# Kernel tuning notes

Hardware: AMD Instinct MI355X
Metric: run time of the kernel (lower is better)

The kernel has to match this reference:

```python
import jax, jax.numpy as jnp
import numpy as np

D_MODEL = 1024
N_HEADS = 16
D_K = D_MODEL // N_HEADS
D_FF = 4096
EPS = 1e-6


def _layernorm(x, g, b):
    mu = jnp.mean(x, axis=-1, keepdims=True)
    var = jnp.mean(jnp.square(x - mu), axis=-1, keepdims=True)
    return (x - mu) * jax.lax.rsqrt(var + EPS) * g + b


def setup_inputs() -> dict:
    key = jax.random.key(0)
    ks = jax.random.split(key, 12)
    B, S = 2, 2048
    sd_attn = (1.0 / np.sqrt(2.0)) * np.sqrt(2.0 / (D_MODEL + D_MODEL))  # xavier gain 1/sqrt(2) (std approx)
    sd_ff1 = np.sqrt(2.0 / (D_MODEL + D_FF))
    sd_ff2 = np.sqrt(2.0 / (D_FF + D_MODEL))
    return {
        "x": jax.random.normal(ks[0], (B, S, D_MODEL), jnp.float32),
        "mask": jnp.ones((B, S), jnp.int32),
        # weights stored (in, out) so forward is x @ W
        "wq": jax.random.normal(ks[1], (D_MODEL, D_MODEL), jnp.float32) * sd_attn,
        "wk": jax.random.normal(ks[2], (D_MODEL, D_MODEL), jnp.float32) * sd_attn,
        "wv": jax.random.normal(ks[3], (D_MODEL, D_MODEL), jnp.float32) * sd_attn,
        "wo": jax.random.normal(ks[4], (D_MODEL, D_MODEL), jnp.float32) * sd_attn,
        "wo_b": jnp.zeros((D_MODEL,), jnp.float32),
        "w1": jax.random.normal(ks[5], (D_MODEL, D_FF), jnp.float32) * sd_ff1,
        "b1": jnp.zeros((D_FF,), jnp.float32),
        "w2": jax.random.normal(ks[6], (D_FF, D_MODEL), jnp.float32) * sd_ff2,
        "b2": jnp.zeros((D_MODEL,), jnp.float32),
        "g1": jnp.ones((D_MODEL,), jnp.float32),
        "be1": jnp.zeros((D_MODEL,), jnp.float32),
        "g2": jnp.ones((D_MODEL,), jnp.float32),
        "be2": jnp.zeros((D_MODEL,), jnp.float32),
    }


def reference(x, mask, wq, wk, wv, wo, wo_b, w1, b1, w2, b2, g1, be1, g2, be2):
    B, S, _ = x.shape
    scale = 1.0 / np.sqrt(D_K)
    # project and split heads -> [B, H, S, Dk]
    q = (x @ wq).reshape(B, S, N_HEADS, D_K).transpose(0, 2, 1, 3)
    k = (x @ wk).reshape(B, S, N_HEADS, D_K).transpose(0, 2, 1, 3)
    v = (x @ wv).reshape(B, S, N_HEADS, D_K).transpose(0, 2, 1, 3)
    scores = jnp.einsum("bhqd,bhkd->bhqk", q, k) * scale  # [B,H,S,S]
    m = (mask[:, None, None, :] == 0)
    scores = jnp.where(m, -1e9, scores)
    attn = jax.nn.softmax(scores, axis=-1)
    ctx = jnp.einsum("bhqk,bhkd->bhqd", attn, v)
    ctx = ctx.transpose(0, 2, 1, 3).reshape(B, S, D_MODEL)
    attn_out = ctx @ wo + wo_b
    x = _layernorm(x + attn_out, g1, be1)
    ff = jax.nn.gelu(x @ w1 + b1, approximate=False) @ w2 + b2
    return _layernorm(x + ff, g2, be2)
```

## Files before the change

kernel.cpp:

```cpp
#include <hip/hip_runtime.h>
#include <cstdint>

#define DEVINL __device__ __forceinline__

typedef __attribute__((ext_vector_type(8))) short short8;
typedef __attribute__((ext_vector_type(4))) float floatx4;
typedef __attribute__((ext_vector_type(4))) unsigned short ushort4v;

DEVINL unsigned short f2bf(float f) {
  union { float f; uint32_t u; } v; v.f = f;
  return (unsigned short)((v.u + 0x7fffu + ((v.u >> 16) & 1u)) >> 16);
}
DEVINL float bf2f(unsigned short h) {
  union { uint32_t u; float f; } v; v.u = ((uint32_t)h) << 16;
  return v.f;
}

#if defined(__has_builtin) && __has_builtin(__builtin_amdgcn_exp2f)
#define EXP2(x) __builtin_amdgcn_exp2f(x)
#else
#define EXP2(x) exp2f(x)
#endif

DEVINL float fast_gelu(float v) {
  const float z = -2.30220795f * v * (1.0f + 0.044715f * v * v);
  return v * __builtin_amdgcn_rcpf(1.0f + EXP2(z));
}

typedef __attribute__((address_space(3))) unsigned char* lds_ptr_t;
typedef const __attribute__((address_space(1))) unsigned char* gbl_ptr_t;
DEVINL void load_lds_128(const void* g, void* l) {
  __builtin_amdgcn_global_load_lds((gbl_ptr_t)g, (lds_ptr_t)l, 16, 0, 0);
}

#define MFMA16(a, b, c) __builtin_amdgcn_mfma_f32_16x16x32_bf16((a), (b), (c), 0, 0, 0)

#define QSCALE2 0.18033688011112042f

__global__ __launch_bounds__(256) void prep_kernel(
    const float* __restrict__ x, unsigned short* __restrict__ XB,
    const float* __restrict__ wq, const float* __restrict__ wk,
    const float* __restrict__ wv, const float* __restrict__ wo,
    unsigned short* __restrict__ WQKV, unsigned short* __restrict__ WOT,
    const float* __restrict__ w1, unsigned short* __restrict__ W1T,
    const float* __restrict__ w2, unsigned short* __restrict__ W2T) {
  const int bid = blockIdx.x;
  if (bid < 4096) {
    const int i = (bid * 256 + threadIdx.x) * 4;
    floatx4 v = *(const floatx4*)(x + i);
    ushort4v o;
#pragma unroll
    for (int j = 0; j < 4; ++j) o[j] = f2bf(v[j]);
    *(ushort4v*)(XB + i) = o;
    return;
  }
  const float* in;
  unsigned short* out;
  int K, N, bx, by;
  if (bid < 8192) {
    const int b2 = bid - 4096, z = b2 >> 10;
    in = (z == 0) ? wq : (z == 1) ? wk : (z == 2) ? wv : wo;
    out = (z == 3) ? WOT : WQKV + (size_t)z * 1024 * 1024;
    K = 1024; N = 1024; bx = b2 & 31; by = (b2 >> 5) & 31;
  } else if (bid < 12288) {
    const int b3 = bid - 8192;
    in = w1; out = W1T; K = 1024; N = 4096; bx = b3 & 127; by = b3 >> 7;
  } else {
    const int b4 = bid - 12288;
    in = w2; out = W2T; K = 4096; N = 1024; bx = b4 & 31; by = b4 >> 5;
  }
  __shared__ float tile[32][33];
  const int n0 = bx * 32, k0 = by * 32;
  const int tx = threadIdx.x & 31, ty = threadIdx.x >> 5;
#pragma unroll
  for (int i = 0; i < 4; ++i)
    tile[ty + 8 * i][tx] = in[(size_t)(k0 + ty + 8 * i) * N + n0 + tx];
  __syncthreads();
#pragma unroll
  for (int i = 0; i < 4; ++i)
    out[(size_t)(n0 + ty + 8 * i) * K + k0 + tx] = f2bf(tile[tx][ty + 8 * i]);
}

template <int EPI, int SK>
__global__ __launch_bounds__(256) void gemm_bt_kernel(
    const unsigned short* __restrict__ A, const unsigned short* __restrict__ BT,
    const float* __restrict__ bias, void* __restrict__ C0, void* __restrict__ C1,
    void* __restrict__ C2, int M, int N, int K) {
  __shared__ __align__(16) unsigned short As[128 * 64];
  __shared__ __align__(16) unsigned short Bs[128 * 64];
  const int tid = threadIdx.x;
  const int w = tid >> 6, l = tid & 63;
  const int lq = l >> 4, lr = l & 15;
  const int m0 = blockIdx.y * 128, n0 = blockIdx.x * 128;
  const int wm = (w >> 1) * 64, wn = (w & 1) * 64;
  const int r_a = l >> 2;
  const int colb = (l & 3) * 8;
  const int kslice = K / SK;
  const int kbeg = kslice * blockIdx.z;

  floatx4 acc[4][4];
  const floatx4 fz = {0.f, 0.f, 0.f, 0.f};
#pragma unroll
  for (int mt = 0; mt < 4; ++mt)
#pragma unroll
    for (int nt = 0; nt < 4; ++nt) acc[mt][nt] = fz;

  for (int k0 = kbeg; k0 < kbeg + kslice; k0 += 64) {
    __syncthreads();
#pragma unroll
    for (int p = 0; p < 2; ++p) {
#pragma unroll
      for (int i = 0; i < 2; ++i) {
        const int c = w * 2 + i;
        load_lds_128(A + (size_t)(m0 + c * 16 + r_a) * K + k0 + p * 32 + colb,
                     (char*)As + p * 8192 + c * 1024);
        load_lds_128(BT + (size_t)(n0 + c * 16 + r_a) * K + k0 + p * 32 + colb,
                     (char*)Bs + p * 8192 + c * 1024);
      }
    }
    __syncthreads();
#pragma unroll
    for (int p = 0; p < 2; ++p) {
      short8 af[4], bf[4];
#pragma unroll
      for (int mt = 0; mt < 4; ++mt)
        af[mt] = *(const short8*)((const char*)As + p * 8192 + (wm + mt * 16 + lr) * 64 + lq * 16);
#pragma unroll
      for (int nt = 0; nt < 4; ++nt)
        bf[nt] = *(const short8*)((const char*)Bs + p * 8192 + (wn + nt * 16 + lr) * 64 + lq * 16);
#pragma unroll
      for (int mt = 0; mt < 4; ++mt)
#pragma unroll
        for (int nt = 0; nt < 4; ++nt)
          acc[mt][nt] = MFMA16(af[mt], bf[nt], acc[mt][nt]);
    }
  }

  void* Cp = (SK > 1 && blockIdx.z) ? C1 : C0;
#pragma unroll
  for (int mt = 0; mt < 4; ++mt) {
#pragma unroll
    for (int nt = 0; nt < 4; ++nt) {
      const int n = n0 + wn + nt * 16 + lr;
      float bval = 0.f;
      if (EPI == 2) bval = bias[n];
#pragma unroll
      for (int r = 0; r < 4; ++r) {
        const int m = m0 + wm + mt * 16 + lq * 4 + r;
        float v = acc[mt][nt][r];
        if (EPI == 4) {
          ((unsigned short*)Cp)[(size_t)m * N + n] = f2bf(v);
        } else if (EPI == 2) {
          ((unsigned short*)C0)[(size_t)m * N + n] = f2bf(fast_gelu(v + bval));
        } else {
          const int reg = n >> 10;
          if (reg == 0) {
            ((unsigned short*)C0)[(size_t)m * 1024 + n] = f2bf(v * QSCALE2);
          } else if (reg == 1) {
            ((unsigned short*)C1)[(size_t)m * 1024 + (n - 1024)] = f2bf(v);
          } else {
            const int nn = n - 2048;
            const int bidx = m >> 11, s = m & 2047;
            const int hh = nn >> 6, d = nn & 63;
            ((unsigned short*)C2)[((size_t)((bidx * 16 + hh) * 64 + d)) * 2048 + s] = f2bf(v);
          }
        }
      }
    }
  }
}

__global__ __launch_bounds__(256, 4) void flash_kernel(
    const unsigned short* __restrict__ Q, const unsigned short* __restrict__ Kg,
    const unsigned short* __restrict__ VT, const int* __restrict__ mask,
    unsigned short* __restrict__ ctx) {
  __shared__ __align__(16) unsigned short Ks[128 * 64];
  __shared__ __align__(16) unsigned short VTs[64 * 128];
  __shared__ __align__(16) unsigned short PQ[64 * 64];

  const int tid = threadIdx.x, w = tid >> 6, l = tid & 63;
  const int lq = l >> 4, lr = l & 15;
  const int bh = blockIdx.y, b = bh >> 4, h = bh & 15;
  const int q0 = blockIdx.x * 64;

  const unsigned short* Qp = Q + (size_t)(b * 2048 + q0) * 1024 + h * 64;
  const unsigned short* Kp = Kg + (size_t)(b * 2048) * 1024 + h * 64;
  const unsigned short* VTp = VT + (size_t)bh * 64 * 2048;
  const int* mp = mask + b * 2048;

  {
    const int rq = l >> 3, cs = l & 7;
#pragma unroll
    for (int i = 0; i < 2; ++i) {
      const int c = w * 2 + i;
      load_lds_128(Qp + (size_t)(c * 8 + rq) * 1024 + cs * 8, (char*)PQ + c * 1024);
    }
  }
  __syncthreads();
  short8 qf[2];
  qf[0] = *(const short8*)((const char*)PQ + (w * 16 + lr) * 128 + lq * 16);
  qf[1] = *(const short8*)((const char*)PQ + (w * 16 + lr) * 128 + 64 + lq * 16);

  short8 ones;
#pragma unroll
  for (int j = 0; j < 8; ++j) ones[j] = (short)0x3F80;

  const floatx4 fz = {0.f, 0.f, 0.f, 0.f};
  floatx4 o[4] = {fz, fz, fz, fz};
  floatx4 l_acc = fz;

  const int krow = l >> 3, kslot = l & 7;
  const int vrow = l >> 4, vslot = l & 15;
  const int pswz = (lr >> 2) & 3;

  for (int kb = 0; kb < 2048; kb += 128) {
    __syncthreads();
#pragma unroll
    for (int i = 0; i < 4; ++i) {
      const int c4 = w * 4 + i;
      {
        const int row = c4 * 8 + krow;
        const int cc = kslot ^ (row & 7);
        load_lds_128(Kp + (size_t)(kb + row) * 1024 + cc * 8, (char*)Ks + c4 * 1024);
      }
      {
        const int row = c4 * 4 + vrow;
        const int cc = vslot ^ (row & 15);
        load_lds_128(VTp + (size_t)row * 2048 + kb + cc * 8, (char*)VTs + c4 * 1024);
      }
    }
    int msk[8];
#pragma unroll
    for (int g = 0; g < 8; ++g) msk[g] = mp[kb + g * 16 + lr];
    __syncthreads();

    floatx4 s[8];
#pragma unroll
    for (int g = 0; g < 8; ++g) {
      const char* rowp = (const char*)Ks + (g * 16 + lr) * 128;
      short8 k0 = *(const short8*)(rowp + ((lq) ^ (lr & 7)) * 16);
      short8 k1 = *(const short8*)(rowp + ((4 + lq) ^ (lr & 7)) * 16);
      floatx4 t = MFMA16(qf[0], k0, fz);
      s[g] = MFMA16(qf[1], k1, t);
    }

    float pH[4][4];
#pragma unroll
    for (int r = 0; r < 4; ++r) {
      unsigned short* pr = PQ + (w * 16 + lq * 4 + r) * 64;
#pragma unroll
      for (int g = 0; g < 4; ++g)
        pr[((g ^ lq) * 16) + lr] = f2bf(msk[g] ? EXP2(s[g][r]) : 0.f);
#pragma unroll
      for (int g = 0; g < 4; ++g)
        pH[r][g] = msk[4 + g] ? EXP2(s[4 + g][r]) : 0.f;
    }

#pragma unroll
    for (int t = 0; t < 2; ++t) {
      short8 pf = *(const short8*)((const char*)PQ + (w * 16 + lr) * 128 +
                                   (((t * 32 + lq * 8) ^ (pswz * 16)) * 2));
      l_acc = MFMA16(pf, ones, l_acc);
#pragma unroll
      for (int nt = 0; nt < 4; ++nt) {
        short8 vf = *(const short8*)((const char*)VTs + (nt * 16 + lr) * 256 +
                                     ((t * 4 + lq) ^ lr) * 16);
        o[nt] = MFMA16(pf, vf, o[nt]);
      }
    }
#pragma unroll
    for (int r = 0; r < 4; ++r) {
      unsigned short* pr = PQ + (w * 16 + lq * 4 + r) * 64;
#pragma unroll
      for (int g = 0; g < 4; ++g) pr[((g ^ lq) * 16) + lr] = f2bf(pH[r][g]);
    }
#pragma unroll
    for (int t = 0; t < 2; ++t) {
      short8 pf = *(const short8*)((const char*)PQ + (w * 16 + lr) * 128 +
                                   (((t * 32 + lq * 8) ^ (pswz * 16)) * 2));
      l_acc = MFMA16(pf, ones, l_acc);
#pragma unroll
      for (int nt = 0; nt < 4; ++nt) {
        short8 vf = *(const short8*)((const char*)VTs + (nt * 16 + lr) * 256 +
                                     ((8 + t * 4 + lq) ^ lr) * 16);
        o[nt] = MFMA16(pf, vf, o[nt]);
      }
    }
  }

#pragma unroll
  for (int r = 0; r < 4; ++r) {
    const float inv = 1.0f / l_acc[r];
    const int q = q0 + w * 16 + lq * 4 + r;
#pragma unroll
    for (int nt = 0; nt < 4; ++nt)
      ctx[(size_t)(b * 2048 + q) * 1024 + h * 64 + nt * 16 + lr] = f2bf(o[nt][r] * inv);
  }
}

template <int RESBF, int OUTBF>
__global__ __launch_bounds__(256) void ln2_kernel(
    const void* __restrict__ res, const unsigned short* __restrict__ y0,
    const unsigned short* __restrict__ y1, const float* __restrict__ bias,
    const float* __restrict__ gamma, const float* __restrict__ beta,
    void* __restrict__ outp) {
  const int row = blockIdx.x, t = threadIdx.x;
  const size_t base = (size_t)row * 1024 + t * 4;
  float v[4];
  if (RESBF) {
    ushort4v r4 = *(const ushort4v*)((const unsigned short*)res + base);
#pragma unroll
    for (int j = 0; j < 4; ++j) v[j] = bf2f(r4[j]);
  } else {
    floatx4 r4 = *(const floatx4*)((const float*)res + base);
#pragma unroll
    for (int j = 0; j < 4; ++j) v[j] = r4[j];
  }
  const ushort4v a4 = *(const ushort4v*)(y0 + base);
  const ushort4v b4v = *(const ushort4v*)(y1 + base);
  const floatx4 bi4 = *(const floatx4*)(bias + t * 4);
  float s = 0.f, ss = 0.f;
#pragma unroll
  for (int j = 0; j < 4; ++j) {
    v[j] += bf2f(a4[j]) + bf2f(b4v[j]) + bi4[j];
    s += v[j];
    ss += v[j] * v[j];
  }
#pragma unroll
  for (int off = 1; off < 64; off <<= 1) {
    s += __shfl_xor(s, off);
    ss += __shfl_xor(ss, off);
  }
  __shared__ float red[8];
  const int w = t >> 6;
  if ((t & 63) == 0) { red[w] = s; red[4 + w] = ss; }
  __syncthreads();
  s = red[0] + red[1] + red[2] + red[3];
  ss = red[4] + red[5] + red[6] + red[7];
  const float mean = s * (1.0f / 1024.0f);
  const float var = ss * (1.0f / 1024.0f) - mean * mean;
  const float rstd = rsqrtf(var + 1e-6f);
  const floatx4 g4 = *(const floatx4*)(gamma + t * 4);
  const floatx4 be4 = *(const floatx4*)(beta + t * 4);
  if (OUTBF) {
    ushort4v o;
#pragma unroll
    for (int j = 0; j < 4; ++j) o[j] = f2bf((v[j] - mean) * rstd * g4[j] + be4[j]);
    *(ushort4v*)((unsigned short*)outp + base) = o;
  } else {
    floatx4 o;
#pragma unroll
    for (int j = 0; j < 4; ++j) o[j] = (v[j] - mean) * rstd * g4[j] + be4[j];
    *(floatx4*)((float*)outp + base) = o;
  }
}

extern "C" void kernel_launch(void* const* d_in, const int* in_sizes, int n_in,
                              void* d_out, int out_size, void* d_ws, size_t ws_size,
                              hipStream_t stream) {
  (void)in_sizes; (void)n_in; (void)out_size; (void)ws_size;
  const float* x    = (const float*)d_in[0];
  const int*   mask = (const int*)d_in[1];
  const float* wq   = (const float*)d_in[2];
  const float* wk   = (const float*)d_in[3];
  const float* wv   = (const float*)d_in[4];
  const float* wo   = (const float*)d_in[5];
  const float* wo_b = (const float*)d_in[6];
  const float* w1   = (const float*)d_in[7];
  const float* b1   = (const float*)d_in[8];
  const float* w2   = (const float*)d_in[9];
  const float* b2   = (const float*)d_in[10];
  const float* g1   = (const float*)d_in[11];
  const float* be1  = (const float*)d_in[12];
  const float* g2   = (const float*)d_in[13];
  const float* be2  = (const float*)d_in[14];
  float* out = (float*)d_out;

  char* ws = (char*)d_ws;
  const size_t MB = 1024ull * 1024ull;
  unsigned short* WQKV = (unsigned short*)(ws + 0 * MB);
  unsigned short* WOT  = (unsigned short*)(ws + 6 * MB);
  unsigned short* W1T  = (unsigned short*)(ws + 8 * MB);
  unsigned short* W2T  = (unsigned short*)(ws + 16 * MB);
  unsigned short* XB   = (unsigned short*)(ws + 24 * MB);
  unsigned short* Qb   = (unsigned short*)(ws + 32 * MB);
  unsigned short* Kb   = (unsigned short*)(ws + 40 * MB);
  unsigned short* VTb  = (unsigned short*)(ws + 48 * MB);
  unsigned short* CTX  = (unsigned short*)(ws + 56 * MB);
  unsigned short* ATT0 = (unsigned short*)(ws + 32 * MB);
  unsigned short* ATT1 = (unsigned short*)(ws + 40 * MB);
  unsigned short* Hb   = (unsigned short*)(ws + 24 * MB);
  unsigned short* G1   = (unsigned short*)(ws + 32 * MB);
  unsigned short* FF20 = (unsigned short*)(ws + 64 * MB);
  unsigned short* FF21 = (unsigned short*)(ws + 72 * MB);

  prep_kernel<<<16384, 256, 0, stream>>>(x, XB, wq, wk, wv, wo, WQKV, WOT,
                                         w1, W1T, w2, W2T);
  gemm_bt_kernel<5, 1><<<dim3(24, 32), 256, 0, stream>>>(
      XB, WQKV, nullptr, Qb, Kb, VTb, 4096, 3072, 1024);
  flash_kernel<<<dim3(32, 32), 256, 0, stream>>>(Qb, Kb, VTb, mask, CTX);
  gemm_bt_kernel<4, 2><<<dim3(8, 32, 2), 256, 0, stream>>>(
      CTX, WOT, nullptr, ATT0, ATT1, nullptr, 4096, 1024, 1024);
  ln2_kernel<0, 1><<<4096, 256, 0, stream>>>(x, ATT0, ATT1, wo_b, g1, be1, Hb);
  gemm_bt_kernel<2, 1><<<dim3(32, 32), 256, 0, stream>>>(
      Hb, W1T, b1, G1, nullptr, nullptr, 4096, 4096, 1024);
  gemm_bt_kernel<4, 2><<<dim3(8, 32, 2), 256, 0, stream>>>(
      G1, W2T, nullptr, FF20, FF21, nullptr, 4096, 1024, 4096);
  ln2_kernel<1, 0><<<4096, 256, 0, stream>>>(Hb, FF20, FF21, b2, g2, be2, out);
}
```

Baseline: 366.2 us.

## Keep softmax probabilities in registers by transposing the score MFMA operands

Swaps the operand order of the QK^T MFMA so each lane's score accumulator already matches the A-operand layout the PV MFMA needs. The probabilities are packed into bf16 fragments in registers, which removes the LDS round trip through the PQ buffer. To fit the new fragment order, V^T is read as two 4-element pieces per fragment and the mask is loaded as int4 vectors. This cuts LDS traffic and shared memory use, but adds more, narrower LDS reads for V and extra register pressure.

```diff
diff --git a/kernel.cpp b/kernel.cpp
--- a/kernel.cpp
+++ b/kernel.cpp
@@ -4,6 +4,7 @@
 #define DEVINL __device__ __forceinline__
 
 typedef __attribute__((ext_vector_type(8))) short short8;
+typedef __attribute__((ext_vector_type(4))) short short4v;
 typedef __attribute__((ext_vector_type(4))) float floatx4;
 typedef __attribute__((ext_vector_type(4))) unsigned short ushort4v;
 
@@ -176,7 +177,6 @@
     unsigned short* __restrict__ ctx) {
   __shared__ __align__(16) unsigned short Ks[128 * 64];
   __shared__ __align__(16) unsigned short VTs[64 * 128];
-  __shared__ __align__(16) unsigned short PQ[64 * 64];
 
   const int tid = threadIdx.x, w = tid >> 6, l = tid & 63;
   const int lq = l >> 4, lr = l & 15;
@@ -193,13 +193,13 @@
 #pragma unroll
     for (int i = 0; i < 2; ++i) {
       const int c = w * 2 + i;
-      load_lds_128(Qp + (size_t)(c * 8 + rq) * 1024 + cs * 8, (char*)PQ + c * 1024);
+      load_lds_128(Qp + (size_t)(c * 8 + rq) * 1024 + cs * 8, (char*)Ks + c * 1024);
     }
   }
   __syncthreads();
   short8 qf[2];
-  qf[0] = *(const short8*)((const char*)PQ + (w * 16 + lr) * 128 + lq * 16);
-  qf[1] = *(const short8*)((const char*)PQ + (w * 16 + lr) * 128 + 64 + lq * 16);
+  qf[0] = *(const short8*)((const char*)Ks + (w * 16 + lr) * 128 + lq * 16);
+  qf[1] = *(const short8*)((const char*)Ks + (w * 16 + lr) * 128 + 64 + lq * 16);
 
   short8 ones;
 #pragma unroll
@@ -211,7 +211,6 @@
 
   const int krow = l >> 3, kslot = l & 7;
   const int vrow = l >> 4, vslot = l & 15;
-  const int pswz = (lr >> 2) & 3;
 
   for (int kb = 0; kb < 2048; kb += 128) {
     __syncthreads();
@@ -229,61 +228,52 @@
         load_lds_128(VTp + (size_t)row * 2048 + kb + cc * 8, (char*)VTs + c4 * 1024);
       }
     }
-    int msk[8];
-#pragma unroll
-    for (int g = 0; g < 8; ++g) msk[g] = mp[kb + g * 16 + lr];
+    int4 msk[8];
+#pragma unroll
+    for (int g = 0; g < 8; ++g) msk[g] = *(const int4*)(mp + kb + g * 16 + lq * 4);
     __syncthreads();
 
-    floatx4 s[8];
-#pragma unroll
-    for (int g = 0; g < 8; ++g) {
-      const char* rowp = (const char*)Ks + (g * 16 + lr) * 128;
-      short8 k0 = *(const short8*)(rowp + ((lq) ^ (lr & 7)) * 16);
-      short8 k1 = *(const short8*)(rowp + ((4 + lq) ^ (lr & 7)) * 16);
-      floatx4 t = MFMA16(qf[0], k0, fz);
-      s[g] = MFMA16(qf[1], k1, t);
-    }
-
-    float pH[4][4];
-#pragma unroll
-    for (int r = 0; r < 4; ++r) {
-      unsigned short* pr = PQ + (w * 16 + lq * 4 + r) * 64;
-#pragma unroll
-      for (int g = 0; g < 4; ++g)
-        pr[((g ^ lq) * 16) + lr] = f2bf(msk[g] ? EXP2(s[g][r]) : 0.f);
-#pragma unroll
-      for (int g = 0; g < 4; ++g)
-        pH[r][g] = msk[4 + g] ? EXP2(s[4 + g][r]) : 0.f;
-    }
-
-#pragma unroll
-    for (int t = 0; t < 2; ++t) {
-      short8 pf = *(const short8*)((const char*)PQ + (w * 16 + lr) * 128 +
-                                   (((t * 32 + lq * 8) ^ (pswz * 16)) * 2));
-      l_acc = MFMA16(pf, ones, l_acc);
-#pragma unroll
-      for (int nt = 0; nt < 4; ++nt) {
-        short8 vf = *(const short8*)((const char*)VTs + (nt * 16 + lr) * 256 +
-                                     ((t * 4 + lq) ^ lr) * 16);
-        o[nt] = MFMA16(pf, vf, o[nt]);
-      }
-    }
-#pragma unroll
-    for (int r = 0; r < 4; ++r) {
-      unsigned short* pr = PQ + (w * 16 + lq * 4 + r) * 64;
-#pragma unroll
-      for (int g = 0; g < 4; ++g) pr[((g ^ lq) * 16) + lr] = f2bf(pH[r][g]);
-    }
-#pragma unroll
-    for (int t = 0; t < 2; ++t) {
-      short8 pf = *(const short8*)((const char*)PQ + (w * 16 + lr) * 128 +
-                                   (((t * 32 + lq * 8) ^ (pswz * 16)) * 2));
-      l_acc = MFMA16(pf, ones, l_acc);
-#pragma unroll
-      for (int nt = 0; nt < 4; ++nt) {
-        short8 vf = *(const short8*)((const char*)VTs + (nt * 16 + lr) * 256 +
-                                     ((8 + t * 4 + lq) ^ lr) * 16);
-        o[nt] = MFMA16(pf, vf, o[nt]);
+#pragma unroll
+    for (int h2 = 0; h2 < 2; ++h2) {
+      floatx4 s[4];
+#pragma unroll
+      for (int gg = 0; gg < 4; ++gg) {
+        const int g = h2 * 4 + gg;
+        const char* rowp = (const char*)Ks + (g * 16 + lr) * 128;
+        short8 k0 = *(const short8*)(rowp + ((lq) ^ (lr & 7)) * 16);
+        short8 k1 = *(const short8*)(rowp + ((4 + lq) ^ (lr & 7)) * 16);
+        floatx4 t = MFMA16(k0, qf[0], fz);
+        s[gg] = MFMA16(k1, qf[1], t);
+      }
+      short8 pf[2];
+#pragma unroll
+      for (int tt = 0; tt < 2; ++tt) {
+        const int4 mL = msk[h2 * 4 + tt * 2], mH = msk[h2 * 4 + tt * 2 + 1];
+        const floatx4 sL = s[tt * 2], sH = s[tt * 2 + 1];
+#pragma unroll
+        for (int j = 0; j < 4; ++j) {
+          float pL, pH;
+          pL = (j == 0 ? mL.x : j == 1 ? mL.y : j == 2 ? mL.z : mL.w) ? EXP2(sL[j]) : 0.f;
+          pH = (j == 0 ? mH.x : j == 1 ? mH.y : j == 2 ? mH.z : mH.w) ? EXP2(sH[j]) : 0.f;
+          pf[tt][j] = (short)f2bf(pL);
+          pf[tt][4 + j] = (short)f2bf(pH);
+        }
+      }
+#pragma unroll
+      for (int tt = 0; tt < 2; ++tt) {
+        const int t = h2 * 2 + tt;
+        l_acc = MFMA16(pf[tt], ones, l_acc);
+        const int kc0 = t * 4 + (lq >> 1);
+        const int off = (lq & 1) * 8;
+#pragma unroll
+        for (int nt = 0; nt < 4; ++nt) {
+          const int d = nt * 16 + lr;
+          const char* vrow_p = (const char*)VTs + d * 256;
+          short4v va = *(const short4v*)(vrow_p + ((kc0 ^ (d & 15)) * 16) + off);
+          short4v vb = *(const short4v*)(vrow_p + (((kc0 + 2) ^ (d & 15)) * 16) + off);
+          short8 vf = {va[0], va[1], va[2], va[3], vb[0], vb[1], vb[2], vb[3]};
+          o[nt] = MFMA16(pf[tt], vf, o[nt]);
+        }
       }
     }
   }
```

Result: faster. 357.4 us (-2.4%).
